# Kernel tuning notes

Hardware: AMD Instinct MI355X
Metric: run time of the kernel (lower is better)

The kernel has to match this reference:

```python
import jax, jax.numpy as jnp
import numpy as np

A = 512   # input channels
B = 32    # number of capsule types
H4 = 16   # h*h pose dims per capsule


def setup_inputs() -> dict:
    key = jax.random.key(0)
    k1, k2, k3, k4, k5 = jax.random.split(key, 5)
    # Input feature map [N, A, H, W]
    x = jax.random.normal(k1, (64, A, 32, 32), dtype=jnp.float32)
    # Fused weights: B parallel 1x1 convs concatenated along out-channel dim.
    # Pose convs: B x Conv2d(A -> 16, k=1) -> [B*16, A]; activation convs: B x Conv2d(A -> 1) -> [B, A]
    bound = 1.0 / np.sqrt(A)  # PyTorch Conv2d default init range
    W_pose = jax.random.uniform(k2, (B * H4, A), minval=-bound, maxval=bound, dtype=jnp.float32)
    b_pose = jax.random.uniform(k3, (B * H4,), minval=-bound, maxval=bound, dtype=jnp.float32)
    W_act = jax.random.uniform(k4, (B, A), minval=-bound, maxval=bound, dtype=jnp.float32)
    b_act = jax.random.uniform(k5, (B,), minval=-bound, maxval=bound, dtype=jnp.float32)
    return {"x": x, "W_pose": W_pose, "b_pose": b_pose, "W_act": W_act, "b_act": b_act}


def reference(x, W_pose, b_pose, W_act, b_act):
    # 1x1 conv == channel contraction; fuse all 2*B tiny convs into two GEMMs.
    # poses: [N, B*16, H, W]
    poses = jnp.einsum('nahw,oa->nohw', x, W_pose) + b_pose[None, :, None, None]
    # activations: sigmoid([N, B, H, W])
    activations = jax.nn.sigmoid(jnp.einsum('nahw,oa->nohw', x, W_act) + b_act[None, :, None, None])
    return poses, activations
```

## Files before the change

kernel.cpp:

```cpp
#include <hip/hip_runtime.h>
#include <hip/hip_bf16.h>


typedef __attribute__((ext_vector_type(8))) short short8;
typedef __attribute__((ext_vector_type(4))) float f32x4;

#define A_CH   512
#define HW     1024
#define N_B    64
#define O_POSE 512
#define O_ACT  32
#define O_TOT  544
#define O_PAD  576
#define TM     32
#define BK     64
#define NIT    (A_CH / BK)
#define NOF    9

__device__ __forceinline__ unsigned pk(float lo, float hi) {
    __hip_bfloat162 h = __float22bfloat162_rn(make_float2(lo, hi));
    return *reinterpret_cast<unsigned*>(&h);
}

__global__ __launch_bounds__(256) void prep_w(const float* __restrict__ Wp,
                                              const float* __restrict__ Wa,
                                              unsigned short* __restrict__ Wb) {
    const int r = blockIdx.x;
    const int c = threadIdx.x * 2;
    float2 v = make_float2(0.f, 0.f);
    if (r < O_POSE)     v = *(const float2*)(Wp + (size_t)r * A_CH + c);
    else if (r < O_TOT) v = *(const float2*)(Wa + (size_t)(r - O_POSE) * A_CH + c);
    __hip_bfloat162 h = __float22bfloat162_rn(v);
    *(unsigned*)(Wb + (size_t)r * A_CH + c) = *reinterpret_cast<unsigned*>(&h);
}

__global__ __launch_bounds__(256, 4) void caps_gemm(
    const float* __restrict__ x,
    const unsigned short* __restrict__ Wb,
    const float* __restrict__ bp,
    const float* __restrict__ ba,
    float* __restrict__ out)
{
    __shared__ __align__(16) short lds[2][TM * BK];

    const int tid = threadIdx.x;
    const int m0  = blockIdx.x * TM;
    const int n   = blockIdx.y;

    const float* xn = x + (size_t)n * A_CH * HW + m0;

    const int sm = tid & 31;
    const int sg = tid >> 5;
    const float* sbase = xn + (size_t)sg * 8 * HW + sm;
    const int wr = sm * BK + ((sg ^ (sm & 7)) << 3);

    float xr[2][8];
    auto load_x = [&](int it, int bank) {
#pragma unroll
        for (int j = 0; j < 8; ++j)
            xr[bank][j] = sbase[(size_t)(it * BK + j) * HW];
    };
    auto store_x = [&](int bank, int buf) {
        short8 v;
#pragma unroll
        for (int j = 0; j < 4; ++j)
            ((unsigned*)&v)[j] = pk(xr[bank][2 * j], xr[bank][2 * j + 1]);
        *(short8*)&lds[buf][wr] = v;
    };

    const int lane = tid & 63;
    const int w    = tid >> 6;
    const int l16  = lane & 15;
    const int g    = lane >> 4;

    const unsigned short* wlane = Wb + (size_t)(w * 144 + l16) * A_CH + g * 8;
    const int bswz = l16 & 7;

    f32x4 acc[NOF][2] = {};

    load_x(0, 0);
    load_x(1, 1);
    store_x(0, 0);
    __syncthreads();

    for (int it = 0; it < NIT; ++it) {
        const int cur = it & 1;
        if (it + 2 < NIT) load_x(it + 2, it & 1);
#pragma unroll
        for (int ks = 0; ks < 2; ++ks) {
            short8 bF[2];
#pragma unroll
            for (int fm = 0; fm < 2; ++fm)
                bF[fm] = *(const short8*)&lds[cur][(fm * 16 + l16) * BK +
                                                   (((ks * 4 + g) ^ bswz) << 3)];
#pragma unroll
            for (int of = 0; of < NOF; ++of) {
                short8 aF = *(const short8*)(wlane + (size_t)of * 16 * A_CH +
                                             it * BK + ks * 32);
#pragma unroll
                for (int fm = 0; fm < 2; ++fm)
                    acc[of][fm] = __builtin_amdgcn_mfma_f32_16x16x32_bf16(
                        aF, bF[fm], acc[of][fm], 0, 0, 0);
            }
        }
        if (it + 1 < NIT) store_x((it + 1) & 1, cur ^ 1);
        __syncthreads();
    }

    float* actOut = out + (size_t)N_B * O_POSE * HW;
    const size_t poseN = (size_t)n * O_POSE * HW;
    const size_t actN  = (size_t)n * O_ACT * HW;
    const int ob = w * 144;
#pragma unroll
    for (int of = 0; of < NOF; ++of) {
#pragma unroll
        for (int i = 0; i < 4; ++i) {
            const int R = ob + of * 16 + g * 4 + i;
            if (R >= O_TOT) continue;
            if (R < O_POSE) {
                const float bias = bp[R];
#pragma unroll
                for (int fm = 0; fm < 2; ++fm) {
                    const int cc = m0 + fm * 16 + l16;
                    __builtin_nontemporal_store(acc[of][fm][i] + bias,
                                                &out[poseN + (size_t)R * HW + cc]);
                }
            } else {
                const float bias = ba[R - O_POSE];
#pragma unroll
                for (int fm = 0; fm < 2; ++fm) {
                    const int cc = m0 + fm * 16 + l16;
                    const float v = acc[of][fm][i] + bias;
                    __builtin_nontemporal_store(1.0f / (1.0f + __expf(-v)),
                                                &actOut[actN + (size_t)(R - O_POSE) * HW + cc]);
                }
            }
        }
    }
}

extern "C" void kernel_launch(void* const* d_in, const int* in_sizes, int n_in,
                              void* d_out, int out_size, void* d_ws, size_t ws_size,
                              hipStream_t stream) {
    (void)in_sizes; (void)n_in; (void)out_size; (void)ws_size;
    const float* x  = (const float*)d_in[0];
    const float* Wp = (const float*)d_in[1];
    const float* bp = (const float*)d_in[2];
    const float* Wa = (const float*)d_in[3];
    const float* ba = (const float*)d_in[4];
    unsigned short* Wb = (unsigned short*)d_ws;

    prep_w<<<dim3(O_PAD), dim3(256), 0, stream>>>(Wp, Wa, Wb);
    caps_gemm<<<dim3(HW / TM, N_B), dim3(256), 0, stream>>>(x, Wb, bp, ba, (float*)d_out);
}
```

Before: 359.0 us.

## Retile GEMM into 128x128 output blocks with LDS-staged weights and XCD-aware mapping

Replaces the per-block full-output-channel tile (weights read directly from global per wave) with 128x128 output tiles over a 5x8x64 grid of 512-thread blocks. Weights are staged into a triple-buffered LDS ring with direct global-to-LDS loads, and x uses BK=32 double buffering with manual waitcnt/barrier. Block indices are remapped so the five channel-blocks sharing an x tile land on the same XCD to reuse x in L2. This trades the earlier redundant per-wave global weight reads for more x re-reads across channel blocks, and wastes compute on padding to 640 output rows.

```diff
diff --git a/kernel.cpp b/kernel.cpp
--- a/kernel.cpp
+++ b/kernel.cpp
@@ -11,15 +11,21 @@
 #define O_POSE 512
 #define O_ACT  32
 #define O_TOT  544
-#define O_PAD  576
-#define TM     32
-#define BK     64
+#define O_PAD  640
+#define TO     128
+#define TM     128
+#define BK     32
 #define NIT    (A_CH / BK)
-#define NOF    9
 
 __device__ __forceinline__ unsigned pk(float lo, float hi) {
     __hip_bfloat162 h = __float22bfloat162_rn(make_float2(lo, hi));
     return *reinterpret_cast<unsigned*>(&h);
+}
+
+__device__ __forceinline__ void glds16(const void* g, void* l) {
+    __builtin_amdgcn_global_load_lds(
+        (const __attribute__((address_space(1))) unsigned*)g,
+        (__attribute__((address_space(3))) unsigned*)l, 16, 0, 0);
 }
 
 __global__ __launch_bounds__(256) void prep_w(const float* __restrict__ Wp,
@@ -34,103 +40,126 @@
     *(unsigned*)(Wb + (size_t)r * A_CH + c) = *reinterpret_cast<unsigned*>(&h);
 }
 
-__global__ __launch_bounds__(256, 4) void caps_gemm(
+__global__ __launch_bounds__(512, 4) void caps_gemm(
     const float* __restrict__ x,
     const unsigned short* __restrict__ Wb,
     const float* __restrict__ bp,
     const float* __restrict__ ba,
     float* __restrict__ out)
 {
-    __shared__ __align__(16) short lds[2][TM * BK];
+    __shared__ __align__(16) short ldsA[3][TO * BK];
+    __shared__ __align__(16) short ldsB[2][TM * BK];
 
     const int tid = threadIdx.x;
-    const int m0  = blockIdx.x * TM;
-    const int n   = blockIdx.y;
 
-    const float* xn = x + (size_t)n * A_CH * HW + m0;
+    const int lin  = blockIdx.x;
+    const int xcd  = lin & 7;
+    const int slot = lin >> 3;
+    const int ob   = slot % 5;
+    const int mnid = (slot / 5) * 8 + xcd;
+    const int m0   = (mnid & 7) * TM;
+    const int n    = mnid >> 3;
+    const int o0   = ob * TO;
 
-    const int sm = tid & 31;
-    const int sg = tid >> 5;
-    const float* sbase = xn + (size_t)sg * 8 * HW + sm;
-    const int wr = sm * BK + ((sg ^ (sm & 7)) << 3);
+    const unsigned short* asrc =
+        Wb + (size_t)(o0 + (tid >> 2)) * A_CH + (((tid & 3) ^ ((tid >> 3) & 3)) * 8);
+
+    const int sm = tid & 127;
+    const int kg = tid >> 7;
+    const float* sbase = x + (size_t)n * A_CH * HW + m0 + sm + (size_t)(kg * 8) * HW;
+    const int xwr = sm * BK + ((kg ^ ((sm >> 1) & 3)) * 8);
 
     float xr[2][8];
-    auto load_x = [&](int it, int bank) {
+
+    const int lane = tid & 63;
+    const int w    = tid >> 6;
+    const int wo   = (w >> 2) * 64;
+    const int wm   = (w & 3) * 32;
+    const int l16  = lane & 15;
+    const int g    = lane >> 4;
+
+    f32x4 acc[4][2] = {};
+
+    glds16(asrc, &ldsA[0][tid * 8]);
 #pragma unroll
-        for (int j = 0; j < 8; ++j)
-            xr[bank][j] = sbase[(size_t)(it * BK + j) * HW];
-    };
-    auto store_x = [&](int bank, int buf) {
+    for (int j = 0; j < 8; ++j) xr[0][j] = sbase[(size_t)j * HW];
+    asm volatile("" ::: "memory");
+    glds16(asrc + BK, &ldsA[1][tid * 8]);
+#pragma unroll
+    for (int j = 0; j < 8; ++j) xr[1][j] = sbase[(size_t)(BK + j) * HW];
+
+    asm volatile("s_waitcnt vmcnt(9)" ::: "memory");
+    {
         short8 v;
 #pragma unroll
         for (int j = 0; j < 4; ++j)
-            ((unsigned*)&v)[j] = pk(xr[bank][2 * j], xr[bank][2 * j + 1]);
-        *(short8*)&lds[buf][wr] = v;
-    };
+            ((unsigned*)&v)[j] = pk(xr[0][2 * j], xr[0][2 * j + 1]);
+        *(short8*)&ldsB[0][xwr] = v;
+    }
+    asm volatile("s_waitcnt lgkmcnt(0)\n\ts_barrier" ::: "memory");
 
-    const int lane = tid & 63;
-    const int w    = tid >> 6;
-    const int l16  = lane & 15;
-    const int g    = lane >> 4;
-
-    const unsigned short* wlane = Wb + (size_t)(w * 144 + l16) * A_CH + g * 8;
-    const int bswz = l16 & 7;
-
-    f32x4 acc[NOF][2] = {};
-
-    load_x(0, 0);
-    load_x(1, 1);
-    store_x(0, 0);
-    __syncthreads();
-
+#pragma unroll
     for (int it = 0; it < NIT; ++it) {
-        const int cur = it & 1;
-        if (it + 2 < NIT) load_x(it + 2, it & 1);
+        if (it + 2 < NIT) {
+            glds16(asrc + (it + 2) * BK, &ldsA[(it + 2) % 3][tid * 8]);
 #pragma unroll
-        for (int ks = 0; ks < 2; ++ks) {
-            short8 bF[2];
+            for (int j = 0; j < 8; ++j)
+                xr[it & 1][j] = sbase[(size_t)((it + 2) * BK + j) * HW];
+        }
+        short8 aF[4], bF[2];
+#pragma unroll
+        for (int f = 0; f < 4; ++f) {
+            const int r = wo + f * 16 + l16;
+            aF[f] = *(const short8*)&ldsA[it % 3][r * BK + ((g ^ ((r >> 1) & 3)) * 8)];
+        }
+#pragma unroll
+        for (int f = 0; f < 2; ++f) {
+            const int c = wm + f * 16 + l16;
+            bF[f] = *(const short8*)&ldsB[it & 1][c * BK + ((g ^ ((c >> 1) & 3)) * 8)];
+        }
+#pragma unroll
+        for (int fo = 0; fo < 4; ++fo)
 #pragma unroll
             for (int fm = 0; fm < 2; ++fm)
-                bF[fm] = *(const short8*)&lds[cur][(fm * 16 + l16) * BK +
-                                                   (((ks * 4 + g) ^ bswz) << 3)];
+                acc[fo][fm] = __builtin_amdgcn_mfma_f32_16x16x32_bf16(
+                    aF[fo], bF[fm], acc[fo][fm], 0, 0, 0);
+        if (it + 1 < NIT) {
+            if (it + 2 < NIT)
+                asm volatile("s_waitcnt vmcnt(9)" ::: "memory");
+            else
+                asm volatile("s_waitcnt vmcnt(0)" ::: "memory");
+            short8 v;
 #pragma unroll
-            for (int of = 0; of < NOF; ++of) {
-                short8 aF = *(const short8*)(wlane + (size_t)of * 16 * A_CH +
-                                             it * BK + ks * 32);
-#pragma unroll
-                for (int fm = 0; fm < 2; ++fm)
-                    acc[of][fm] = __builtin_amdgcn_mfma_f32_16x16x32_bf16(
-                        aF, bF[fm], acc[of][fm], 0, 0, 0);
-            }
+            for (int j = 0; j < 4; ++j)
+                ((unsigned*)&v)[j] = pk(xr[(it + 1) & 1][2 * j], xr[(it + 1) & 1][2 * j + 1]);
+            *(short8*)&ldsB[(it + 1) & 1][xwr] = v;
+            asm volatile("s_waitcnt lgkmcnt(0)\n\ts_barrier" ::: "memory");
         }
-        if (it + 1 < NIT) store_x((it + 1) & 1, cur ^ 1);
-        __syncthreads();
     }
 
     float* actOut = out + (size_t)N_B * O_POSE * HW;
     const size_t poseN = (size_t)n * O_POSE * HW;
     const size_t actN  = (size_t)n * O_ACT * HW;
-    const int ob = w * 144;
 #pragma unroll
-    for (int of = 0; of < NOF; ++of) {
+    for (int fo = 0; fo < 4; ++fo) {
 #pragma unroll
         for (int i = 0; i < 4; ++i) {
-            const int R = ob + of * 16 + g * 4 + i;
+            const int R = o0 + wo + fo * 16 + g * 4 + i;
             if (R >= O_TOT) continue;
             if (R < O_POSE) {
                 const float bias = bp[R];
 #pragma unroll
                 for (int fm = 0; fm < 2; ++fm) {
-                    const int cc = m0 + fm * 16 + l16;
-                    __builtin_nontemporal_store(acc[of][fm][i] + bias,
+                    const int cc = m0 + wm + fm * 16 + l16;
+                    __builtin_nontemporal_store(acc[fo][fm][i] + bias,
                                                 &out[poseN + (size_t)R * HW + cc]);
                 }
             } else {
                 const float bias = ba[R - O_POSE];
 #pragma unroll
                 for (int fm = 0; fm < 2; ++fm) {
-                    const int cc = m0 + fm * 16 + l16;
-                    const float v = acc[of][fm][i] + bias;
+                    const int cc = m0 + wm + fm * 16 + l16;
+                    const float v = acc[fo][fm][i] + bias;
                     __builtin_nontemporal_store(1.0f / (1.0f + __expf(-v)),
                                                 &actOut[actN + (size_t)(R - O_POSE) * HW + cc]);
                 }
@@ -151,5 +180,5 @@
     unsigned short* Wb = (unsigned short*)d_ws;
 
     prep_w<<<dim3(O_PAD), dim3(256), 0, stream>>>(Wp, Wa, Wb);
-    caps_gemm<<<dim3(HW / TM, N_B), dim3(256), 0, stream>>>(x, Wb, bp, ba, (float*)d_out);
+    caps_gemm<<<dim3(8 * 5 * N_B), dim3(512), 0, stream>>>(x, Wb, bp, ba, (float*)d_out);
 }
```

After: 296.4 us. -17.4%, faster.
